# Kernel tuning notes

Hardware: AMD Instinct MI355X
Metric: run time of the kernel (lower is better)

Reference implementation:

```python
import jax, jax.numpy as jnp
import numpy as np

B, E, H = 32768, 512, 512


def setup_inputs() -> dict:
    key = jax.random.key(0)
    ks = jax.random.split(key, 7)
    s_e = 1.0 / np.sqrt(E)
    s_h = 1.0 / np.sqrt(H)
    return {
        "input": jax.random.normal(ks[0], (B, E), jnp.float32),
        "h0": jax.random.normal(ks[1], (B, H), jnp.float32),
        "c0": jax.random.normal(ks[2], (B, H), jnp.float32),
        # stacked weights, gate order [i, f, o, g]
        "W_x": jax.random.uniform(ks[3], (4, H, E), jnp.float32, -s_e, s_e),
        "b_x": jax.random.uniform(ks[4], (4, H), jnp.float32, -s_e, s_e),
        "W_h": jax.random.uniform(ks[5], (4, H, H), jnp.float32, -s_h, s_h),
        "b_h": jax.random.uniform(ks[6], (4, H), jnp.float32, -s_h, s_h),
    }


def reference(input, h0, c0, W_x, b_x, W_h, b_h):
    # Fused: two GEMMs over stacked gate weights, then elementwise gate math.
    # z: [4, B, H]; gate order i, f, o, g
    z = (jnp.einsum('be,khe->kbh', input, W_x) + b_x[:, None, :]
         + jnp.einsum('bh,kgh->kbg', h0, W_h) + b_h[:, None, :])
    i = jax.nn.sigmoid(z[0])
    f = jax.nn.sigmoid(z[1])
    o = jax.nn.sigmoid(z[2])
    g = jnp.tanh(z[3])
    c1 = f * c0 + i * g
    h1 = o * jnp.tanh(c1)
    return (h1, c1)
```

## Files before the change

kernel.cpp:

```cpp
#include <hip/hip_runtime.h>
#include <hip/hip_bf16.h>


#define BQ 32768
#define HQ 512
#define KK 1024
#define BH (32768 * 512)

typedef __bf16 bf16x8 __attribute__((ext_vector_type(8)));
typedef float f32x4 __attribute__((ext_vector_type(4)));

__device__ __forceinline__ unsigned short f2bf(float f) {
    unsigned int u = __float_as_uint(f);
    unsigned int r = (u + 0x7fffu + ((u >> 16) & 1u)) >> 16;
    return (unsigned short)r;
}

__device__ __forceinline__ void gld_lds16(const unsigned short* g, unsigned short* l) {
    __builtin_amdgcn_global_load_lds(
        (const __attribute__((address_space(1))) void*)g,
        (__attribute__((address_space(3))) void*)l,
        16, 0, 0);
}


__global__ __launch_bounds__(256) void pack_X(const float* __restrict__ in,
                                              const float* __restrict__ h0,
                                              unsigned short* __restrict__ Xcat) {
    const int NQ = BQ * HQ / 4;
    int gi = blockIdx.x * 256 + threadIdx.x;
    const float* src;
    size_t dst;
    if (gi < NQ) {
        int e = gi * 4;
        int b = e >> 9, col = e & 511;
        src = in + e;
        dst = (size_t)b * 1024 + col;
    } else {
        int e = (gi - NQ) * 4;
        int b = e >> 9, col = e & 511;
        src = h0 + e;
        dst = (size_t)b * 1024 + 512 + col;
    }
    float4 v = *(const float4*)src;
    ushort4 o;
    o.x = f2bf(v.x); o.y = f2bf(v.y); o.z = f2bf(v.z); o.w = f2bf(v.w);
    *(ushort4*)&Xcat[dst] = o;
}

__global__ __launch_bounds__(256) void pack_W(const float* __restrict__ Wx,
                                              const float* __restrict__ Wh,
                                              const float* __restrict__ bx,
                                              const float* __restrict__ bh,
                                              unsigned short* __restrict__ Wint,
                                              float* __restrict__ biasc) {
    int j = blockIdx.x * 256 + threadIdx.x;
    int c = j >> 8;
    int kc = (j & 255) * 4;
    int gate = (c >> 4) & 3;
    int h = ((c >> 6) << 4) + (c & 15);
    const float* src = (kc < 512)
        ? (Wx + ((size_t)gate * 512 + h) * 512 + kc)
        : (Wh + ((size_t)gate * 512 + h) * 512 + (kc - 512));
    float4 v = *(const float4*)src;
    ushort4 o;
    o.x = f2bf(v.x); o.y = f2bf(v.y); o.z = f2bf(v.z); o.w = f2bf(v.w);
    *(ushort4*)&Wint[(size_t)c * 1024 + kc] = o;
    if ((j & 255) == 0) biasc[c] = bx[gate * 512 + h] + bh[gate * 512 + h];
}


__global__ __launch_bounds__(256) void lstm_gemm(const unsigned short* __restrict__ Xcat,
                                                 const unsigned short* __restrict__ Wint,
                                                 const float* __restrict__ biasc,
                                                 const float* __restrict__ c0,
                                                 float* __restrict__ out) {
    __shared__ __align__(16) unsigned short ldsA[128 * 32];
    __shared__ __align__(16) unsigned short ldsB[128 * 32];

    const int tid = threadIdx.x;
    const int lane = tid & 63;
    const int wave = tid >> 6;
    const int wm = wave >> 1;
    const int wn = wave & 1;
    const int quad = lane >> 4;
    const int lrow = lane & 15;
    const int koff = quad * 8;

    const int bn = blockIdx.x;
    const int bm = blockIdx.y;
    const int m0 = bm * 128;
    const int n0 = bn * 128;

    const int arow = tid >> 2;
    const int acol = (tid & 3) * 8;

    f32x4 acc[4][4];
    for (int i = 0; i < 4; i++)
        for (int j = 0; j < 4; j++) {
            f32x4 z = {0.f, 0.f, 0.f, 0.f};
            acc[i][j] = z;
        }

    const unsigned short* gA = Xcat + (size_t)(m0 + arow) * KK + acol;
    const unsigned short* gB = Wint + (size_t)(n0 + arow) * KK + acol;

    for (int kt = 0; kt < KK; kt += 32) {
        gld_lds16(gA + kt, &ldsA[tid * 8]);
        gld_lds16(gA + (size_t)64 * KK + kt, &ldsA[2048 + tid * 8]);
        gld_lds16(gB + kt, &ldsB[tid * 8]);
        gld_lds16(gB + (size_t)64 * KK + kt, &ldsB[2048 + tid * 8]);
        __syncthreads();

        bf16x8 af[4], bfr[4];
        for (int mi = 0; mi < 4; mi++)
            af[mi] = *(const bf16x8*)&ldsA[(wm * 64 + mi * 16 + lrow) * 32 + koff];
        for (int ni = 0; ni < 4; ni++)
            bfr[ni] = *(const bf16x8*)&ldsB[(wn * 64 + ni * 16 + lrow) * 32 + koff];
        for (int mi = 0; mi < 4; mi++)
            for (int ni = 0; ni < 4; ni++)
                acc[mi][ni] = __builtin_amdgcn_mfma_f32_16x16x32_bf16(
                    af[mi], bfr[ni], acc[mi][ni], 0, 0, 0);
        __syncthreads();
    }

    float bi[4];
    for (int ni = 0; ni < 4; ni++)
        bi[ni] = biasc[n0 + wn * 64 + ni * 16 + lrow];
    const int h = (bn * 2 + wn) * 16 + lrow;

    for (int mi = 0; mi < 4; mi++) {
        for (int r = 0; r < 4; r++) {
            int b = m0 + wm * 64 + mi * 16 + quad * 4 + r;
            float zi = acc[mi][0][r] + bi[0];
            float zf = acc[mi][1][r] + bi[1];
            float zo = acc[mi][2][r] + bi[2];
            float zg = acc[mi][3][r] + bi[3];
            float ig = 1.f / (1.f + __expf(-zi));
            float fg = 1.f / (1.f + __expf(-zf));
            float og = 1.f / (1.f + __expf(-zo));
            float gg = 1.f - 2.f / (__expf(2.f * zg) + 1.f);
            float c0v = c0[(size_t)b * HQ + h];
            float c1 = fg * c0v + ig * gg;
            float th = 1.f - 2.f / (__expf(2.f * c1) + 1.f);
            out[(size_t)b * HQ + h] = og * th;
            out[(size_t)BH + (size_t)b * HQ + h] = c1;
        }
    }
}

extern "C" void kernel_launch(void* const* d_in, const int* in_sizes, int n_in,
                              void* d_out, int out_size, void* d_ws, size_t ws_size,
                              hipStream_t stream) {
    (void)in_sizes; (void)n_in; (void)out_size; (void)ws_size;
    const float* input = (const float*)d_in[0];
    const float* h0    = (const float*)d_in[1];
    const float* c0    = (const float*)d_in[2];
    const float* Wx    = (const float*)d_in[3];
    const float* bx    = (const float*)d_in[4];
    const float* Wh    = (const float*)d_in[5];
    const float* bh    = (const float*)d_in[6];
    float* out = (float*)d_out;

    char* ws = (char*)d_ws;
    unsigned short* Xcat = (unsigned short*)ws;
    unsigned short* Wint = (unsigned short*)(ws + (size_t)67108864);
    float* biasc = (float*)(ws + (size_t)71303168);

    pack_X<<<32768, 256, 0, stream>>>(input, h0, Xcat);
    pack_W<<<2048, 256, 0, stream>>>(Wx, Wh, bx, bh, Wint, biasc);
    lstm_gemm<<<dim3(16, 256), 256, 0, stream>>>(Xcat, Wint, biasc, c0, out);
}
```

Measured before the change: 474.2 us.

## Fuse fp32-to-bf16 activation conversion into GEMM and swizzle LDS layout

Drops the separate pack_X kernel. The GEMM now loads fp32 input and h0 rows directly, converts them to bf16 in registers, and stores them into LDS, prefetching the next k-tile into registers while the current one computes. LDS writes and reads for A and B use an XOR swizzle to reduce bank conflicts, and launch bounds request 4 blocks per CU. This avoids writing and re-reading a 64MB bf16 staging buffer and one kernel launch. In exchange, each A tile is reconverted by all 16 column blocks, which means more fp32 global traffic (A reads double in bytes) and more register pressure.

```diff
diff --git a/kernel.cpp b/kernel.cpp
--- a/kernel.cpp
+++ b/kernel.cpp
@@ -1,5 +1,4 @@
 #include <hip/hip_runtime.h>
-#include <hip/hip_bf16.h>
 
 
 #define BQ 32768
@@ -23,30 +22,13 @@
         16, 0, 0);
 }
 
+__device__ __forceinline__ bf16x8 cvt8(f32x4 a, f32x4 b) {
+    bf16x8 w;
+    w[0] = (__bf16)a[0]; w[1] = (__bf16)a[1]; w[2] = (__bf16)a[2]; w[3] = (__bf16)a[3];
+    w[4] = (__bf16)b[0]; w[5] = (__bf16)b[1]; w[6] = (__bf16)b[2]; w[7] = (__bf16)b[3];
+    return w;
+}
 
-__global__ __launch_bounds__(256) void pack_X(const float* __restrict__ in,
-                                              const float* __restrict__ h0,
-                                              unsigned short* __restrict__ Xcat) {
-    const int NQ = BQ * HQ / 4;
-    int gi = blockIdx.x * 256 + threadIdx.x;
-    const float* src;
-    size_t dst;
-    if (gi < NQ) {
-        int e = gi * 4;
-        int b = e >> 9, col = e & 511;
-        src = in + e;
-        dst = (size_t)b * 1024 + col;
-    } else {
-        int e = (gi - NQ) * 4;
-        int b = e >> 9, col = e & 511;
-        src = h0 + e;
-        dst = (size_t)b * 1024 + 512 + col;
-    }
-    float4 v = *(const float4*)src;
-    ushort4 o;
-    o.x = f2bf(v.x); o.y = f2bf(v.y); o.z = f2bf(v.z); o.w = f2bf(v.w);
-    *(ushort4*)&Xcat[dst] = o;
-}
 
 __global__ __launch_bounds__(256) void pack_W(const float* __restrict__ Wx,
                                               const float* __restrict__ Wh,
@@ -70,11 +52,12 @@
 }
 
 
-__global__ __launch_bounds__(256) void lstm_gemm(const unsigned short* __restrict__ Xcat,
-                                                 const unsigned short* __restrict__ Wint,
-                                                 const float* __restrict__ biasc,
-                                                 const float* __restrict__ c0,
-                                                 float* __restrict__ out) {
+__global__ __launch_bounds__(256, 4) void lstm_gemm(const float* __restrict__ xin,
+                                                    const float* __restrict__ hin,
+                                                    const unsigned short* __restrict__ Wint,
+                                                    const float* __restrict__ biasc,
+                                                    const float* __restrict__ c0,
+                                                    float* __restrict__ out) {
     __shared__ __align__(16) unsigned short ldsA[128 * 32];
     __shared__ __align__(16) unsigned short ldsB[128 * 32];
 
@@ -85,15 +68,25 @@
     const int wn = wave & 1;
     const int quad = lane >> 4;
     const int lrow = lane & 15;
-    const int koff = quad * 8;
 
     const int bn = blockIdx.x;
     const int bm = blockIdx.y;
     const int m0 = bm * 128;
     const int n0 = bn * 128;
 
-    const int arow = tid >> 2;
-    const int acol = (tid & 3) * 8;
+    const int arow = tid >> 1;
+    const int ahalf = tid & 1;
+    const int aswz = (arow >> 1) & 3;
+    const float* gAx = xin + (size_t)(m0 + arow) * HQ + ahalf * 16;
+    const float* gAh = hin + (size_t)(m0 + arow) * HQ + ahalf * 16;
+    unsigned short* wA0 = &ldsA[arow * 32 + (((ahalf * 2 + 0) ^ aswz) * 8)];
+    unsigned short* wA1 = &ldsA[arow * 32 + (((ahalf * 2 + 1) ^ aswz) * 8)];
+
+    const int brow = tid >> 2;
+    const int bunit = (tid & 3) ^ ((tid >> 3) & 3);
+    const unsigned short* gB = Wint + (size_t)(n0 + brow) * KK + bunit * 8;
+
+    const int koff = (quad ^ ((lrow >> 1) & 3)) * 8;
 
     f32x4 acc[4][4];
     for (int i = 0; i < 4; i++)
@@ -102,15 +95,26 @@
             acc[i][j] = z;
         }
 
-    const unsigned short* gA = Xcat + (size_t)(m0 + arow) * KK + acol;
-    const unsigned short* gB = Wint + (size_t)(n0 + arow) * KK + acol;
+    f32x4 r0 = *(const f32x4*)(gAx + 0);
+    f32x4 r1 = *(const f32x4*)(gAx + 4);
+    f32x4 r2 = *(const f32x4*)(gAx + 8);
+    f32x4 r3 = *(const f32x4*)(gAx + 12);
 
     for (int kt = 0; kt < KK; kt += 32) {
-        gld_lds16(gA + kt, &ldsA[tid * 8]);
-        gld_lds16(gA + (size_t)64 * KK + kt, &ldsA[2048 + tid * 8]);
         gld_lds16(gB + kt, &ldsB[tid * 8]);
         gld_lds16(gB + (size_t)64 * KK + kt, &ldsB[2048 + tid * 8]);
+        *(bf16x8*)wA0 = cvt8(r0, r1);
+        *(bf16x8*)wA1 = cvt8(r2, r3);
         __syncthreads();
+
+        const int kn = kt + 32;
+        if (kn < KK) {
+            const float* p = (kn < 512) ? (gAx + kn) : (gAh + (kn - 512));
+            r0 = *(const f32x4*)(p + 0);
+            r1 = *(const f32x4*)(p + 4);
+            r2 = *(const f32x4*)(p + 8);
+            r3 = *(const f32x4*)(p + 12);
+        }
 
         bf16x8 af[4], bfr[4];
         for (int mi = 0; mi < 4; mi++)
@@ -163,11 +167,9 @@
     float* out = (float*)d_out;
 
     char* ws = (char*)d_ws;
-    unsigned short* Xcat = (unsigned short*)ws;
-    unsigned short* Wint = (unsigned short*)(ws + (size_t)67108864);
-    float* biasc = (float*)(ws + (size_t)71303168);
+    unsigned short* Wint = (unsigned short*)ws;
+    float* biasc = (float*)(ws + (size_t)4 * 1024 * 1024);
 
-    pack_X<<<32768, 256, 0, stream>>>(input, h0, Xcat);
     pack_W<<<2048, 256, 0, stream>>>(Wx, Wh, bx, bh, Wint, biasc);
-    lstm_gemm<<<dim3(16, 256), 256, 0, stream>>>(Xcat, Wint, biasc, c0, out);
+    lstm_gemm<<<dim3(16, 256), 256, 0, stream>>>(input, h0, Wint, biasc, c0, out);
 }
```

Measured after the change: 503.3 us. +6.1%, slower.

## Triple-buffer LDS pipeline with 256x128 tiles, XOR swizzle and block remap

Applied to the files above, without the earlier changes.

Rewrites the GEMM main loop as a three-stage global_load_lds pipeline over 64-wide K steps, with manual vmcnt waits and raw barriers in place of the double __syncthreads per step. Block tile grows to 256x128 with 512 threads (8 waves), an XOR swizzle is applied to LDS columns to cut bank conflicts, and block IDs are remapped for L2 locality. It also raises MFMA priority with s_setprio. This costs much more LDS per block (144 KB), and the hand-placed waitcnt counts must exactly match the number of outstanding loads.

```diff
diff --git a/kernel.cpp b/kernel.cpp
--- a/kernel.cpp
+++ b/kernel.cpp
@@ -1,5 +1,4 @@
 #include <hip/hip_runtime.h>
-#include <hip/hip_bf16.h>
 
 
 #define BQ 32768
@@ -70,13 +69,13 @@
 }
 
 
-__global__ __launch_bounds__(256) void lstm_gemm(const unsigned short* __restrict__ Xcat,
-                                                 const unsigned short* __restrict__ Wint,
-                                                 const float* __restrict__ biasc,
-                                                 const float* __restrict__ c0,
-                                                 float* __restrict__ out) {
-    __shared__ __align__(16) unsigned short ldsA[128 * 32];
-    __shared__ __align__(16) unsigned short ldsB[128 * 32];
+__global__ __launch_bounds__(512, 2) void lstm_gemm(const unsigned short* __restrict__ Xcat,
+                                                    const unsigned short* __restrict__ Wint,
+                                                    const float* __restrict__ biasc,
+                                                    const float* __restrict__ c0,
+                                                    float* __restrict__ out) {
+    __shared__ __align__(16) unsigned short ldsA[3][2][256 * 32];
+    __shared__ __align__(16) unsigned short ldsB[3][2][128 * 32];
 
     const int tid = threadIdx.x;
     const int lane = tid & 63;
@@ -85,51 +84,118 @@
     const int wn = wave & 1;
     const int quad = lane >> 4;
     const int lrow = lane & 15;
-    const int koff = quad * 8;
-
-    const int bn = blockIdx.x;
-    const int bm = blockIdx.y;
-    const int m0 = bm * 128;
+
+    const int bid = blockIdx.x;
+    const int l = bid >> 3;
+    const int bm = (bid & 7) * 16 + (l >> 4);
+    const int bn = l & 15;
+    const int m0 = bm * 256;
     const int n0 = bn * 128;
 
-    const int arow = tid >> 2;
-    const int acol = (tid & 3) * 8;
+    const int trow = tid >> 2;
+    const int aunit = ((tid & 3) ^ ((tid >> 3) & 3)) * 8;
+    const int t8 = tid * 8;
+    const unsigned short* gA0 = Xcat + (size_t)(m0 + trow) * KK + aunit;
+    const unsigned short* gA1 = gA0 + (size_t)128 * KK;
+    const unsigned short* gB0 = Wint + (size_t)(n0 + trow) * KK + aunit;
+
+    const int koff = (quad ^ ((lrow >> 1) & 3)) * 8;
 
     f32x4 acc[4][4];
+#pragma unroll
     for (int i = 0; i < 4; i++)
+#pragma unroll
         for (int j = 0; j < 4; j++) {
             f32x4 z = {0.f, 0.f, 0.f, 0.f};
             acc[i][j] = z;
         }
 
-    const unsigned short* gA = Xcat + (size_t)(m0 + arow) * KK + acol;
-    const unsigned short* gB = Wint + (size_t)(n0 + arow) * KK + acol;
-
-    for (int kt = 0; kt < KK; kt += 32) {
-        gld_lds16(gA + kt, &ldsA[tid * 8]);
-        gld_lds16(gA + (size_t)64 * KK + kt, &ldsA[2048 + tid * 8]);
-        gld_lds16(gB + kt, &ldsB[tid * 8]);
-        gld_lds16(gB + (size_t)64 * KK + kt, &ldsB[2048 + tid * 8]);
-        __syncthreads();
-
-        bf16x8 af[4], bfr[4];
-        for (int mi = 0; mi < 4; mi++)
-            af[mi] = *(const bf16x8*)&ldsA[(wm * 64 + mi * 16 + lrow) * 32 + koff];
-        for (int ni = 0; ni < 4; ni++)
-            bfr[ni] = *(const bf16x8*)&ldsB[(wn * 64 + ni * 16 + lrow) * 32 + koff];
-        for (int mi = 0; mi < 4; mi++)
+#pragma unroll
+    for (int tt = 0; tt < 2; ++tt) {
+        const int kt = tt * 64;
+        gld_lds16(gA0 + kt,      &ldsA[tt][0][t8]);
+        gld_lds16(gA1 + kt,      &ldsA[tt][0][4096 + t8]);
+        gld_lds16(gB0 + kt,      &ldsB[tt][0][t8]);
+        gld_lds16(gA0 + kt + 32, &ldsA[tt][1][t8]);
+        gld_lds16(gA1 + kt + 32, &ldsA[tt][1][4096 + t8]);
+        gld_lds16(gB0 + kt + 32, &ldsB[tt][1][t8]);
+    }
+    asm volatile("s_waitcnt vmcnt(6)" ::: "memory");
+    __builtin_amdgcn_s_barrier();
+
+    int bufR = 0;
+    int bufS = 2;
+
+    for (int T = 0; T < 16; ++T) {
+        const int kt2 = T * 64 + 128;
+        const bool st = (T < 14);
+
+        {
+            bf16x8 af[4], bfr[4];
+#pragma unroll
+            for (int mi = 0; mi < 4; mi++)
+                af[mi] = *(const bf16x8*)&ldsA[bufR][0][(wm * 64 + mi * 16 + lrow) * 32 + koff];
+#pragma unroll
             for (int ni = 0; ni < 4; ni++)
-                acc[mi][ni] = __builtin_amdgcn_mfma_f32_16x16x32_bf16(
-                    af[mi], bfr[ni], acc[mi][ni], 0, 0, 0);
-        __syncthreads();
+                bfr[ni] = *(const bf16x8*)&ldsB[bufR][0][(wn * 64 + ni * 16 + lrow) * 32 + koff];
+            if (st) {
+                gld_lds16(gA0 + kt2, &ldsA[bufS][0][t8]);
+                gld_lds16(gA1 + kt2, &ldsA[bufS][0][4096 + t8]);
+                gld_lds16(gB0 + kt2, &ldsB[bufS][0][t8]);
+            }
+            __builtin_amdgcn_s_barrier();
+            __builtin_amdgcn_s_setprio(1);
+#pragma unroll
+            for (int mi = 0; mi < 4; mi++)
+#pragma unroll
+                for (int ni = 0; ni < 4; ni++)
+                    acc[mi][ni] = __builtin_amdgcn_mfma_f32_16x16x32_bf16(
+                        af[mi], bfr[ni], acc[mi][ni], 0, 0, 0);
+            __builtin_amdgcn_s_setprio(0);
+            __builtin_amdgcn_s_barrier();
+        }
+
+        {
+            bf16x8 af[4], bfr[4];
+#pragma unroll
+            for (int mi = 0; mi < 4; mi++)
+                af[mi] = *(const bf16x8*)&ldsA[bufR][1][(wm * 64 + mi * 16 + lrow) * 32 + koff];
+#pragma unroll
+            for (int ni = 0; ni < 4; ni++)
+                bfr[ni] = *(const bf16x8*)&ldsB[bufR][1][(wn * 64 + ni * 16 + lrow) * 32 + koff];
+            if (st) {
+                gld_lds16(gA0 + kt2 + 32, &ldsA[bufS][1][t8]);
+                gld_lds16(gA1 + kt2 + 32, &ldsA[bufS][1][4096 + t8]);
+                gld_lds16(gB0 + kt2 + 32, &ldsB[bufS][1][t8]);
+                asm volatile("s_waitcnt vmcnt(6)" ::: "memory");
+            } else {
+                asm volatile("s_waitcnt vmcnt(0)" ::: "memory");
+            }
+            __builtin_amdgcn_s_barrier();
+            __builtin_amdgcn_s_setprio(1);
+#pragma unroll
+            for (int mi = 0; mi < 4; mi++)
+#pragma unroll
+                for (int ni = 0; ni < 4; ni++)
+                    acc[mi][ni] = __builtin_amdgcn_mfma_f32_16x16x32_bf16(
+                        af[mi], bfr[ni], acc[mi][ni], 0, 0, 0);
+            __builtin_amdgcn_s_setprio(0);
+            __builtin_amdgcn_s_barrier();
+        }
+
+        bufR = (bufR == 2) ? 0 : bufR + 1;
+        bufS = (bufS == 2) ? 0 : bufS + 1;
     }
 
     float bi[4];
+#pragma unroll
     for (int ni = 0; ni < 4; ni++)
         bi[ni] = biasc[n0 + wn * 64 + ni * 16 + lrow];
     const int h = (bn * 2 + wn) * 16 + lrow;
 
+#pragma unroll
     for (int mi = 0; mi < 4; mi++) {
+#pragma unroll
         for (int r = 0; r < 4; r++) {
             int b = m0 + wm * 64 + mi * 16 + quad * 4 + r;
             float zi = acc[mi][0][r] + bi[0];
@@ -169,5 +235,5 @@
 
     pack_X<<<32768, 256, 0, stream>>>(input, h0, Xcat);
     pack_W<<<2048, 256, 0, stream>>>(Wx, Wh, bx, bh, Wint, biasc);
-    lstm_gemm<<<dim3(16, 256), 256, 0, stream>>>(Xcat, Wint, biasc, c0, out);
-}
+    lstm_gemm<<<2048, 512, 0, stream>>>(Xcat, Wint, biasc, c0, out);
+}
```

New measurement: 476.4 us. Within noise of the previous version (+0.5%).

## Rewrite LSTM GEMM with 256x256 tiles, double-buffered LDS, swizzle and phased MFMA

Applied to the files above, without the earlier changes.

The main GEMM kernel moves from 128x128 tiles with single-buffered LDS and two barriers per k-step to 256x256 tiles with 8 waves, K=64 per stage, double-buffered LDS, XOR-swizzled LDS layout, and split A/B prefetch interleaved with MFMA clusters under setprio. The block index is remapped for L2 locality. The aim is to hide global load latency, remove LDS bank conflicts and raise arithmetic intensity per byte loaded. The cost is higher register pressure from 128 accumulator floats per lane and 128 KB of LDS per block, which limits occupancy.

```diff
diff --git a/kernel.cpp b/kernel.cpp
--- a/kernel.cpp
+++ b/kernel.cpp
@@ -1,5 +1,4 @@
 #include <hip/hip_runtime.h>
-#include <hip/hip_bf16.h>
 
 
 #define BQ 32768
@@ -70,68 +69,138 @@
 }
 
 
-__global__ __launch_bounds__(256) void lstm_gemm(const unsigned short* __restrict__ Xcat,
-                                                 const unsigned short* __restrict__ Wint,
-                                                 const float* __restrict__ biasc,
-                                                 const float* __restrict__ c0,
-                                                 float* __restrict__ out) {
-    __shared__ __align__(16) unsigned short ldsA[128 * 32];
-    __shared__ __align__(16) unsigned short ldsB[128 * 32];
+__global__ __launch_bounds__(512, 2) void lstm_gemm(const unsigned short* __restrict__ Xcat,
+                                                    const unsigned short* __restrict__ Wint,
+                                                    const float* __restrict__ biasc,
+                                                    const float* __restrict__ c0,
+                                                    float* __restrict__ out) {
+    __shared__ __align__(16) unsigned short ldsA[2][256 * 64];
+    __shared__ __align__(16) unsigned short ldsB[2][256 * 64];
 
     const int tid = threadIdx.x;
     const int lane = tid & 63;
     const int wave = tid >> 6;
-    const int wm = wave >> 1;
-    const int wn = wave & 1;
+    const int wm = wave >> 2;
+    const int wn = wave & 3;
     const int quad = lane >> 4;
     const int lrow = lane & 15;
-    const int koff = quad * 8;
-
-    const int bn = blockIdx.x;
-    const int bm = blockIdx.y;
-    const int m0 = bm * 128;
-    const int n0 = bn * 128;
-
-    const int arow = tid >> 2;
-    const int acol = (tid & 3) * 8;
-
-    f32x4 acc[4][4];
-    for (int i = 0; i < 4; i++)
+
+    const int bid = blockIdx.x;
+    const int l = bid >> 3;
+    const int bm = (bid & 7) * 16 + (l >> 3);
+    const int bn = l & 7;
+    const int m0 = bm * 256;
+    const int n0 = bn * 256;
+
+    const int srow = tid >> 3;
+    const int scol = ((tid & 7) ^ (srow & 7)) * 8;
+    const unsigned short* pA = Xcat + (size_t)(m0 + srow) * KK + scol;
+    const unsigned short* pB = Wint + (size_t)(n0 + srow) * KK + scol;
+
+    const int ro = lrow * 64;
+    const int u0 = ((quad)     ^ (lrow & 7)) * 8;
+    const int u1 = ((quad + 4) ^ (lrow & 7)) * 8;
+    const int ab = (wm * 128) * 64 + ro;
+    const int bb = (wn * 64) * 64 + ro;
+
+    f32x4 acc[8][4];
+#pragma unroll
+    for (int i = 0; i < 8; i++)
+#pragma unroll
         for (int j = 0; j < 4; j++) {
             f32x4 z = {0.f, 0.f, 0.f, 0.f};
             acc[i][j] = z;
         }
 
-    const unsigned short* gA = Xcat + (size_t)(m0 + arow) * KK + acol;
-    const unsigned short* gB = Wint + (size_t)(n0 + arow) * KK + acol;
-
-    for (int kt = 0; kt < KK; kt += 32) {
-        gld_lds16(gA + kt, &ldsA[tid * 8]);
-        gld_lds16(gA + (size_t)64 * KK + kt, &ldsA[2048 + tid * 8]);
-        gld_lds16(gB + kt, &ldsB[tid * 8]);
-        gld_lds16(gB + (size_t)64 * KK + kt, &ldsB[2048 + tid * 8]);
-        __syncthreads();
-
-        bf16x8 af[4], bfr[4];
-        for (int mi = 0; mi < 4; mi++)
-            af[mi] = *(const bf16x8*)&ldsA[(wm * 64 + mi * 16 + lrow) * 32 + koff];
-        for (int ni = 0; ni < 4; ni++)
-            bfr[ni] = *(const bf16x8*)&ldsB[(wn * 64 + ni * 16 + lrow) * 32 + koff];
-        for (int mi = 0; mi < 4; mi++)
-            for (int ni = 0; ni < 4; ni++)
-                acc[mi][ni] = __builtin_amdgcn_mfma_f32_16x16x32_bf16(
-                    af[mi], bfr[ni], acc[mi][ni], 0, 0, 0);
-        __syncthreads();
+#define STAGE_A(Tt, nb) do { const size_t ko_ = (size_t)(Tt) * 64;             \
+    gld_lds16(pA + ko_,                       &ldsA[nb][(0 * 512 + tid) * 8]); \
+    gld_lds16(pA + 64 * (size_t)KK + ko_,     &ldsA[nb][(1 * 512 + tid) * 8]); \
+    gld_lds16(pA + 128 * (size_t)KK + ko_,    &ldsA[nb][(2 * 512 + tid) * 8]); \
+    gld_lds16(pA + 192 * (size_t)KK + ko_,    &ldsA[nb][(3 * 512 + tid) * 8]); \
+} while (0)
+#define STAGE_B(Tt, nb) do { const size_t ko_ = (size_t)(Tt) * 64;             \
+    gld_lds16(pB + ko_,                       &ldsB[nb][(0 * 512 + tid) * 8]); \
+    gld_lds16(pB + 64 * (size_t)KK + ko_,     &ldsB[nb][(1 * 512 + tid) * 8]); \
+    gld_lds16(pB + 128 * (size_t)KK + ko_,    &ldsB[nb][(2 * 512 + tid) * 8]); \
+    gld_lds16(pB + 192 * (size_t)KK + ko_,    &ldsB[nb][(3 * 512 + tid) * 8]); \
+} while (0)
+
+#define CLUSTER(MH, NH) do {                                                   \
+    __builtin_amdgcn_s_setprio(1);                                             \
+    _Pragma("unroll")                                                          \
+    for (int mi = 0; mi < 4; mi++) {                                           \
+        _Pragma("unroll")                                                      \
+        for (int gg = 0; gg < 2; gg++) {                                       \
+            const int g = (NH) * 2 + gg;                                       \
+            acc[(MH) * 4 + mi][g] = __builtin_amdgcn_mfma_f32_16x16x32_bf16(   \
+                af[mi][0], bfr[g][0], acc[(MH) * 4 + mi][g], 0, 0, 0);         \
+            acc[(MH) * 4 + mi][g] = __builtin_amdgcn_mfma_f32_16x16x32_bf16(   \
+                af[mi][1], bfr[g][1], acc[(MH) * 4 + mi][g], 0, 0, 0);         \
+        }                                                                      \
+    }                                                                          \
+    __builtin_amdgcn_s_setprio(0);                                             \
+} while (0)
+
+    STAGE_A(0, 0);
+    STAGE_B(0, 0);
+
+#pragma unroll 2
+    for (int T = 0; T < 16; ++T) {
+        const int cur = T & 1;
+        if (T < 15) {
+            STAGE_A(T + 1, cur ^ 1);
+            asm volatile("s_waitcnt vmcnt(4)" ::: "memory");
+        } else {
+            asm volatile("s_waitcnt vmcnt(0)" ::: "memory");
+        }
+        __builtin_amdgcn_s_barrier();
+        __builtin_amdgcn_sched_barrier(0);
+
+        bf16x8 af[4][2], bfr[4][2];
+#pragma unroll
+        for (int g = 0; g < 4; g++) {
+            bfr[g][0] = *(const bf16x8*)&ldsB[cur][bb + (g * 16) * 64 + u0];
+            bfr[g][1] = *(const bf16x8*)&ldsB[cur][bb + (g * 16) * 64 + u1];
+        }
+#pragma unroll
+        for (int mi = 0; mi < 4; mi++) {
+            af[mi][0] = *(const bf16x8*)&ldsA[cur][ab + (mi * 16) * 64 + u0];
+            af[mi][1] = *(const bf16x8*)&ldsA[cur][ab + (mi * 16) * 64 + u1];
+        }
+
+        CLUSTER(0, 0);
+        __builtin_amdgcn_s_barrier();
+        CLUSTER(0, 1);
+        __builtin_amdgcn_s_barrier();
+
+#pragma unroll
+        for (int mi = 0; mi < 4; mi++) {
+            af[mi][0] = *(const bf16x8*)&ldsA[cur][ab + (64 + mi * 16) * 64 + u0];
+            af[mi][1] = *(const bf16x8*)&ldsA[cur][ab + (64 + mi * 16) * 64 + u1];
+        }
+        if (T < 15) STAGE_B(T + 1, cur ^ 1);
+        __builtin_amdgcn_s_barrier();
+
+        CLUSTER(1, 0);
+        __builtin_amdgcn_s_barrier();
+        CLUSTER(1, 1);
+        __builtin_amdgcn_s_barrier();
     }
+#undef STAGE_A
+#undef STAGE_B
+#undef CLUSTER
 
     float bi[4];
-    for (int ni = 0; ni < 4; ni++)
-        bi[ni] = biasc[n0 + wn * 64 + ni * 16 + lrow];
-    const int h = (bn * 2 + wn) * 16 + lrow;
-
-    for (int mi = 0; mi < 4; mi++) {
+#pragma unroll
+    for (int g = 0; g < 4; g++)
+        bi[g] = biasc[n0 + wn * 64 + g * 16 + lrow];
+    const int h = (bn * 4 + wn) * 16 + lrow;
+
+#pragma unroll
+    for (int mi = 0; mi < 8; mi++) {
+#pragma unroll
         for (int r = 0; r < 4; r++) {
-            int b = m0 + wm * 64 + mi * 16 + quad * 4 + r;
+            int b = m0 + wm * 128 + mi * 16 + quad * 4 + r;
             float zi = acc[mi][0][r] + bi[0];
             float zf = acc[mi][1][r] + bi[1];
             float zo = acc[mi][2][r] + bi[2];
@@ -169,5 +238,5 @@
 
     pack_X<<<32768, 256, 0, stream>>>(input, h0, Xcat);
     pack_W<<<2048, 256, 0, stream>>>(Wx, Wh, bx, bh, Wint, biasc);
-    lstm_gemm<<<dim3(16, 256), 256, 0, stream>>>(Xcat, Wint, biasc, c0, out);
-}
+    lstm_gemm<<<1024, 512, 0, stream>>>(Xcat, Wint, biasc, c0, out);
+}
```

Result: faster. 427.5 us (-9.8%).
